# Kernel optimization log

Hardware: AMD Instinct MI355X
Metric: run time of the kernel (lower is better)

Reference implementation:

```python
import jax, jax.numpy as jnp
from jax import lax
import numpy as np

B, H, W, D_MODEL = 2, 64, 64, 192
D_INNER, D_STATE, DT_RANK = 384, 16, 12
L = H * W
LN_EPS = 1e-5


def setup_inputs() -> dict:
    ks = jax.random.split(jax.random.key(0), 12)
    rng = np.random.default_rng(0)
    perm = rng.permutation(L).astype(np.int32)

    def p(i, shape, scale=0.02):
        return jax.random.normal(ks[i], shape, dtype=jnp.float32) * scale

    return {
        "x": jax.random.normal(ks[0], (B, H, W, D_MODEL), dtype=jnp.float32),
        "condition": jax.random.normal(ks[1], (B, H, W, D_MODEL), dtype=jnp.float32),
        "W_in": p(2, (2 * D_INNER, D_MODEL)),
        "W_con": p(3, (D_INNER, D_MODEL)),
        "conv_w": p(4, (D_INNER, 1, 3, 3)),
        "conv_b": jnp.zeros((D_INNER,), jnp.float32),
        "con_conv_w": p(5, (D_INNER, 1, 3, 3)),
        "con_conv_b": jnp.zeros((D_INNER,), jnp.float32),
        "x_proj_w": p(6, (DT_RANK + 2 * D_STATE, D_INNER)),
        "dt_proj_w": p(7, (D_INNER, DT_RANK)),
        "dt_proj_b": p(8, (D_INNER,), 0.1),
        "A_logs": jnp.tile(jnp.log(jnp.arange(1, D_STATE + 1, dtype=jnp.float32))[None, :], (D_INNER, 1)),
        "Ds": jnp.ones((D_INNER,), jnp.float32),
        "ln_w": jnp.ones((D_INNER,), jnp.float32),
        "ln_b": jnp.zeros((D_INNER,), jnp.float32),
        "W_out": p(9, (D_MODEL, D_INNER)),
        "scan_path": jnp.asarray(perm),
        "rev_scan_path": jnp.asarray(np.argsort(perm).astype(np.int32)),
    }


def _dwconv(x, w, b):
    # depthwise 3x3 conv, SAME padding; x: [B, C, H, W], w: [C, 1, 3, 3]
    y = lax.conv_general_dilated(x, w, (1, 1), "SAME",
                                 dimension_numbers=("NCHW", "OIHW", "NCHW"),
                                 feature_group_count=x.shape[1])
    return y + b[None, :, None, None]


def _selective_scan(u, delta, A, Bs, Cs, D):
    # u, delta: [B, D, L]; A: [D, N]; Bs, Cs: [B, N, L]; D: [D]
    dA = jnp.exp(jnp.einsum("bdl,dn->lbdn", delta, A))          # [L, B, D, N]
    dBu = jnp.einsum("bdl,bnl,bdl->lbdn", delta, Bs, u)          # [L, B, D, N]
    Ct = jnp.transpose(Cs, (2, 0, 1))                             # [L, B, N]
    h0 = jnp.zeros(dA.shape[1:], dA.dtype)

    def step(h, inp):
        a, b, c = inp
        h = a * h + b
        return h, jnp.einsum("bdn,bn->bd", h, c)

    _, ys = lax.scan(step, h0, (dA, dBu, Ct))                     # ys: [L, B, D]
    y = jnp.transpose(ys, (1, 2, 0))                              # [B, D, L]
    return y + u * D[None, :, None]


def _forward(x, condition, W_in, W_con, conv_w, conv_b, con_conv_w, con_conv_b,
             x_proj_w, dt_proj_w, dt_proj_b, A_logs, Ds, ln_w, ln_b, W_out,
             scan_path, rev_scan_path):
    b, h, w, _ = x.shape
    l = h * w
    xz = x @ W_in.T                                               # [B, H, W, 2*Din]
    xa, z = jnp.split(xz, 2, axis=-1)
    z = jax.nn.silu(z)
    c = condition @ W_con.T
    xa = jax.nn.silu(_dwconv(jnp.transpose(xa, (0, 3, 1, 2)), conv_w, conv_b))
    c = jax.nn.silu(_dwconv(jnp.transpose(c, (0, 3, 1, 2)), con_conv_w, con_conv_b))
    d = xa.shape[1]
    xs = xa.reshape(b, d, l)[:, :, scan_path]                     # forward_permutation, K=1
    cs = c.reshape(b, d, l)[:, :, scan_path]
    x_dbl = jnp.einsum("bdl,cd->bcl", xs + cs, x_proj_w)          # [B, R+2N, L]
    r, n = dt_proj_w.shape[1], A_logs.shape[1]
    dts = jnp.einsum("brl,dr->bdl", x_dbl[:, :r], dt_proj_w)
    Bs = x_dbl[:, r:r + n]
    Cs = x_dbl[:, r + n:]
    A = -jnp.exp(A_logs)
    delta = jax.nn.softplus(dts + dt_proj_b[None, :, None])       # delta_softplus=True
    y = _selective_scan(xs, delta, A, Bs, Cs, Ds)                 # [B, D, L]
    y = y[:, :, rev_scan_path]                                    # backward_permutation
    y = jnp.transpose(y, (0, 2, 1))                               # [B, L, D]
    mu = jnp.mean(y, axis=-1, keepdims=True)
    var = jnp.var(y, axis=-1, keepdims=True)
    y = (y - mu) * lax.rsqrt(var + LN_EPS) * ln_w + ln_b          # out_norm
    y = y.reshape(b, h, w, d) * z
    return y @ W_out.T                                            # out_proj (no bias)


def reference(x, condition, W_in, W_con, conv_w, conv_b, con_conv_w, con_conv_b,
              x_proj_w, dt_proj_w, dt_proj_b, A_logs, Ds, ln_w, ln_b, W_out,
              scan_path, rev_scan_path):
    return _forward(x, condition, W_in, W_con, conv_w, conv_b, con_conv_w,
                    con_conv_b, x_proj_w, dt_proj_w, dt_proj_b, A_logs, Ds,
                    ln_w, ln_b, W_out, scan_path, rev_scan_path)
```

## Files before the change

kernel.cpp:

```cpp
#include <hip/hip_runtime.h>
#include <math.h>

#define BB 2
#define HH 64
#define WW 64
#define DM 192
#define DI 384
#define NS 16
#define DTR 12
#define LL 4096
#define ROWS (BB*LL)
#define NCHUNK 128
#define LCHUNK 32
#define NCOMB 448
#define CSTRIDE ((size_t)BB * DI * 8)

typedef __attribute__((ext_vector_type(8))) short bf16x8;
typedef __attribute__((ext_vector_type(4))) float f32x4;

typedef __attribute__((address_space(3))) void        as3_void;
typedef __attribute__((address_space(1))) const void  as1_cvoid;

__device__ __forceinline__ void gl_lds16(const unsigned short* g, unsigned short* l) {
    __builtin_amdgcn_global_load_lds((as1_cvoid*)g, (as3_void*)l, 16, 0, 0);
}

#define WAITCNT_BARRIER(N)                                         \
    do {                                                           \
        asm volatile("s_waitcnt vmcnt(" #N ")" ::: "memory");      \
        __builtin_amdgcn_s_barrier();                              \
        asm volatile("" ::: "memory");                             \
    } while (0)

__device__ __forceinline__ float silu_f(float v) {
    return v / (1.0f + __expf(-v));
}

__device__ __forceinline__ unsigned short f2bf(float f) {
    union { float f; unsigned int u; } c; c.f = f;
    unsigned int u = c.u;
    u += 0x7fffu + ((u >> 16) & 1u);
    return (unsigned short)(u >> 16);
}
__device__ __forceinline__ float bf2f(unsigned short h) {
    union { unsigned int u; float f; } c; c.u = ((unsigned int)h) << 16;
    return c.f;
}

__device__ __forceinline__ bf16x8 f2bf8(float4 a, float4 b) {
    bf16x8 r;
    r[0] = (short)f2bf(a.x); r[1] = (short)f2bf(a.y);
    r[2] = (short)f2bf(a.z); r[3] = (short)f2bf(a.w);
    r[4] = (short)f2bf(b.x); r[5] = (short)f2bf(b.y);
    r[6] = (short)f2bf(b.z); r[7] = (short)f2bf(b.w);
    return r;
}

__global__ __launch_bounds__(256) void gemm_in(
    const float* __restrict__ x, const float* __restrict__ cond,
    const float* __restrict__ w_in, const float* __restrict__ w_con,
    const float* __restrict__ x_proj_w, const float* __restrict__ dt_w,
    const float* __restrict__ w_out,
    unsigned short* __restrict__ xa_bf, unsigned short* __restrict__ z_bf,
    unsigned short* __restrict__ c_bf,
    unsigned short* __restrict__ wcomb_bf, unsigned short* __restrict__ w_out_bf)
{
    const int y = blockIdx.y;
    __shared__ __align__(16) unsigned short sA[2 * 64 * 32];
    __shared__ __align__(16) unsigned short sB[2 * 64 * 32];

    if (y == 18) {
        const int base = blockIdx.x * 256 + threadIdx.x;
        for (int i = base; i < 18432; i += 32768) {
            float4 v = ((const float4*)w_out)[i];
            ushort4 o;
            o.x = f2bf(v.x); o.y = f2bf(v.y); o.z = f2bf(v.z); o.w = f2bf(v.w);
            ((ushort4*)w_out_bf)[i] = o;
        }
        for (int e = base; e < NCOMB * DI; e += 32768) {
            int row = e / DI, k = e - row * DI;
            float v = 0.f;
            if (row < 384) {
                const float* dw = dt_w + row * DTR;
                #pragma unroll
                for (int r = 0; r < DTR; ++r) v += dw[r] * x_proj_w[r * DI + k];
            } else if (row < 416) {
                v = x_proj_w[(12 + (row - 384)) * DI + k];
            }
            wcomb_bf[e] = f2bf(v);
        }
        return;
    }

    const int zz = (y >= 12) ? 1 : 0;
    const float* A = zz ? cond : x;
    const float* W = zz ? w_con : w_in;
    const int bn = (zz ? (y - 12) : y) * 64;
    const int bm = blockIdx.x * 64;

    const int tid  = threadIdx.x;
    const int wave = tid >> 6;
    const int lane = tid & 63;
    const int quad = lane >> 4;
    const int l16  = lane & 15;
    const int srow = tid >> 2;
    const int q4   = tid & 3;
    const int wcol = (q4 ^ ((srow >> 1) & 3)) * 8;
    const int rswz = (quad ^ ((l16 >> 1) & 3)) * 8;

    f32x4 acc[4];
    #pragma unroll
    for (int t = 0; t < 4; ++t) acc[t] = (f32x4)(0.f);

    const float* gA = &A[(size_t)(bm + srow) * DM + q4 * 8];
    const float* gB = &W[(size_t)(bn + srow) * DM + q4 * 8];

    float4 ra0 = *(const float4*)gA,        ra1 = *(const float4*)(gA + 4);
    float4 rb0 = *(const float4*)gB,        rb1 = *(const float4*)(gB + 4);
    *(bf16x8*)&sA[srow * 32 + wcol] = f2bf8(ra0, ra1);
    *(bf16x8*)&sB[srow * 32 + wcol] = f2bf8(rb0, rb1);
    ra0 = *(const float4*)(gA + 32); ra1 = *(const float4*)(gA + 36);
    rb0 = *(const float4*)(gB + 32); rb1 = *(const float4*)(gB + 36);

    const int ar = (wave * 16 + l16) * 32 + rswz;

    #pragma unroll
    for (int t = 0; t < 6; ++t) {
        __syncthreads();
        const unsigned short* cA = &sA[(t & 1) * 2048];
        const unsigned short* cB = &sB[(t & 1) * 2048];
        bf16x8 a = *(bf16x8*)&cA[ar];
        if (t + 1 < 6) {
            const int nb = (t + 1) & 1;
            *(bf16x8*)&sA[nb * 2048 + srow * 32 + wcol] = f2bf8(ra0, ra1);
            *(bf16x8*)&sB[nb * 2048 + srow * 32 + wcol] = f2bf8(rb0, rb1);
            if (t + 2 < 6) {
                const int k = (t + 2) * 32;
                ra0 = *(const float4*)(gA + k); ra1 = *(const float4*)(gA + k + 4);
                rb0 = *(const float4*)(gB + k); rb1 = *(const float4*)(gB + k + 4);
            }
        }
        #pragma unroll
        for (int n = 0; n < 4; ++n) {
            bf16x8 b = *(bf16x8*)&cB[(n * 16 + l16) * 32 + rswz];
            acc[n] = __builtin_amdgcn_mfma_f32_16x16x32_bf16(a, b, acc[n], 0, 0, 0);
        }
    }

    #pragma unroll
    for (int n = 0; n < 4; ++n) {
        int col = bn + n * 16 + l16;
        #pragma unroll
        for (int r = 0; r < 4; ++r) {
            int row = bm + wave * 16 + quad * 4 + r;
            float v = acc[n][r];
            if (zz == 0) {
                if (col < 384) xa_bf[(size_t)row * 384 + col] = f2bf(v);
                else           z_bf[(size_t)row * 384 + (col - 384)] = f2bf(silu_f(v));
            } else {
                c_bf[(size_t)row * 384 + col] = f2bf(v);
            }
        }
    }
}

__global__ __launch_bounds__(256) void gemm_comb(
    const unsigned short* __restrict__ A, const unsigned short* __restrict__ W,
    const float* __restrict__ bias, float* __restrict__ btct,
    unsigned short* __restrict__ du_lo)
{
    __shared__ __align__(16) unsigned short sA[4 * 64 * 32];
    __shared__ __align__(16) unsigned short sB[4 * 64 * 32];
    const int bm = blockIdx.x * 64;
    const int bn = blockIdx.y * 64;
    const int tid  = threadIdx.x;
    const int wave = tid >> 6;
    const int lane = tid & 63;
    const int quad = lane >> 4;
    const int l16  = lane & 15;
    const int srow = tid >> 2;
    const int scol = ((tid & 3) ^ ((tid >> 3) & 3)) * 8;
    const int rswz = (quad ^ ((l16 >> 1) & 3)) * 8;

    f32x4 acc[4];
    #pragma unroll
    for (int t = 0; t < 4; ++t) acc[t] = (f32x4)(0.f);

    const unsigned short* gA = &A[(size_t)(bm + srow) * DI + scol];
    const unsigned short* gB = &W[(size_t)(bn + srow) * DI + scol];

    #pragma unroll
    for (int p = 0; p < 3; ++p) {
        gl_lds16(gA + p * 32, &sA[p * 2048 + wave * 512]);
        gl_lds16(gB + p * 32, &sB[p * 2048 + wave * 512]);
    }
    WAITCNT_BARRIER(4);

    const int ar = (wave * 16 + l16) * 32 + rswz;

    #pragma unroll
    for (int t = 0; t < 12; ++t) {
        if (t + 3 < 12) {
            const int k = (t + 3) * 32, pb = (t + 3) & 3;
            gl_lds16(gA + k, &sA[pb * 2048 + wave * 512]);
            gl_lds16(gB + k, &sB[pb * 2048 + wave * 512]);
        }
        const unsigned short* cA = &sA[(t & 3) * 2048];
        const unsigned short* cB = &sB[(t & 3) * 2048];
        bf16x8 a = *(bf16x8*)&cA[ar];
        #pragma unroll
        for (int n = 0; n < 4; ++n) {
            bf16x8 b = *(bf16x8*)&cB[(n * 16 + l16) * 32 + rswz];
            acc[n] = __builtin_amdgcn_mfma_f32_16x16x32_bf16(a, b, acc[n], 0, 0, 0);
        }
        if (t < 11) {
            if (t + 3 < 12)      WAITCNT_BARRIER(4);
            else if (t + 2 < 12) WAITCNT_BARRIER(2);
            else                 WAITCNT_BARRIER(0);
        }
    }

    #pragma unroll
    for (int n = 0; n < 4; ++n) {
        int col = bn + n * 16 + l16;
        #pragma unroll
        for (int r = 0; r < 4; ++r) {
            int row = bm + wave * 16 + quad * 4 + r;
            float v = acc[n][r];
            if (col < 384) {
                float a = v + bias[col];
                float sp = (a > 20.f) ? a : log1pf(__expf(a));
                du_lo[((size_t)row * 384 + col) * 2] = f2bf(sp);
            } else if (col < 416) {
                int idx = col - 384;
                int pos = (idx < 16) ? ((idx & 7) * 4 + (idx >> 3))
                                     : (((idx - 16) & 7) * 4 + 2 + ((idx - 16) >> 3));
                btct[(size_t)row * 32 + pos] = v;
            }
        }
    }
}

__global__ __launch_bounds__(256) void gemm_out_fused(
    const unsigned short* __restrict__ yt, const unsigned short* __restrict__ z,
    const float* __restrict__ ln_w, const float* __restrict__ ln_b,
    const unsigned short* __restrict__ W, float* __restrict__ out)
{
    __shared__ __align__(16) unsigned short sA[32 * 392];
    const int bm = blockIdx.x * 32;
    const int bn = blockIdx.y * 64;
    const int tid = threadIdx.x;
    const int r2  = tid >> 3;
    const int q8  = tid & 7;
    const int b   = bm >> 12;
    const int l   = (bm & (LL - 1)) + r2;

    const unsigned short* yrow = yt + ((size_t)(b * LL + l)) * DI;
    const unsigned short* zrow = z  + ((size_t)(b * LL + l)) * DI;

    bf16x8 yv[6];
    float s = 0.f, s2 = 0.f;
    #pragma unroll
    for (int i = 0; i < 6; ++i) {
        yv[i] = *(const bf16x8*)&yrow[i * 64 + q8 * 8];
        #pragma unroll
        for (int e = 0; e < 8; ++e) {
            float f = bf2f((unsigned short)yv[i][e]);
            s += f; s2 += f * f;
        }
    }
    s  += __shfl_xor(s, 1);  s  += __shfl_xor(s, 2);  s  += __shfl_xor(s, 4);
    s2 += __shfl_xor(s2, 1); s2 += __shfl_xor(s2, 2); s2 += __shfl_xor(s2, 4);
    const float mu  = s * (1.0f / DI);
    const float inv = rsqrtf(s2 * (1.0f / DI) - mu * mu + 1e-5f);

    #pragma unroll
    for (int i = 0; i < 6; ++i) {
        int c = i * 64 + q8 * 8;
        bf16x8 zv = *(const bf16x8*)&zrow[c];
        float4 wa = *(const float4*)&ln_w[c];
        float4 wb = *(const float4*)&ln_w[c + 4];
        float4 ba = *(const float4*)&ln_b[c];
        float4 bb = *(const float4*)&ln_b[c + 4];
        bf16x8 o;
        o[0] = (short)f2bf(((bf2f((unsigned short)yv[i][0]) - mu) * inv * wa.x + ba.x) * bf2f((unsigned short)zv[0]));
        o[1] = (short)f2bf(((bf2f((unsigned short)yv[i][1]) - mu) * inv * wa.y + ba.y) * bf2f((unsigned short)zv[1]));
        o[2] = (short)f2bf(((bf2f((unsigned short)yv[i][2]) - mu) * inv * wa.z + ba.z) * bf2f((unsigned short)zv[2]));
        o[3] = (short)f2bf(((bf2f((unsigned short)yv[i][3]) - mu) * inv * wa.w + ba.w) * bf2f((unsigned short)zv[3]));
        o[4] = (short)f2bf(((bf2f((unsigned short)yv[i][4]) - mu) * inv * wb.x + bb.x) * bf2f((unsigned short)zv[4]));
        o[5] = (short)f2bf(((bf2f((unsigned short)yv[i][5]) - mu) * inv * wb.y + bb.y) * bf2f((unsigned short)zv[5]));
        o[6] = (short)f2bf(((bf2f((unsigned short)yv[i][6]) - mu) * inv * wb.z + bb.z) * bf2f((unsigned short)zv[6]));
        o[7] = (short)f2bf(((bf2f((unsigned short)yv[i][7]) - mu) * inv * wb.w + bb.w) * bf2f((unsigned short)zv[7]));
        *(bf16x8*)&sA[r2 * 392 + c] = o;
    }

    __syncthreads();

    const int wave = tid >> 6;
    const int lane = tid & 63;
    const int quad = lane >> 4;
    const int l16  = lane & 15;
    const int rf   = wave >> 1;
    const int np   = (wave & 1) * 2;

    f32x4 acc[2];
    acc[0] = (f32x4)(0.f); acc[1] = (f32x4)(0.f);

    const unsigned short* bp0 = &W[(size_t)(bn + np * 16 + l16) * DI + quad * 8];
    const unsigned short* bp1 = bp0 + (size_t)16 * DI;
    const int abase = (rf * 16 + l16) * 392 + quad * 8;

    #pragma unroll
    for (int t = 0; t < 12; ++t) {
        bf16x8 a  = *(bf16x8*)&sA[abase + t * 32];
        bf16x8 b0 = *(const bf16x8*)(bp0 + t * 32);
        bf16x8 b1 = *(const bf16x8*)(bp1 + t * 32);
        acc[0] = __builtin_amdgcn_mfma_f32_16x16x32_bf16(a, b0, acc[0], 0, 0, 0);
        acc[1] = __builtin_amdgcn_mfma_f32_16x16x32_bf16(a, b1, acc[1], 0, 0, 0);
    }

    #pragma unroll
    for (int k = 0; k < 2; ++k) {
        int col = bn + (np + k) * 16 + l16;
        #pragma unroll
        for (int rr = 0; rr < 4; ++rr) {
            int row = bm + rf * 16 + quad * 4 + rr;
            out[(size_t)row * DM + col] = acc[k][rr];
        }
    }
}

__global__ __launch_bounds__(256) void dwconv2_scatter(
    const unsigned short* __restrict__ xin, const unsigned short* __restrict__ cin,
    const float* __restrict__ wx, const float* __restrict__ bx,
    const float* __restrict__ wc, const float* __restrict__ bc,
    const int* __restrict__ rev_scan_path,
    unsigned short* __restrict__ du_hi,
    unsigned short* __restrict__ s_bf)
{
    const int tile = blockIdx.x;
    const int c0   = blockIdx.y * 32;
    const int b    = blockIdx.z;
    const int h0 = (tile >> 3) * 8, w0 = (tile & 7) * 8;
    __shared__ float smx[10 * 10 * 32];
    __shared__ float smc[10 * 10 * 32];
    __shared__ int   jtile[64];

    for (int idx = threadIdx.x; idx < 800; idx += 256) {
        int pix = idx >> 3, cq = (idx & 7) * 4;
        int py = pix / 10, px = pix - py * 10;
        int gh = h0 + py - 1, gw = w0 + px - 1;
        float4 fx = make_float4(0.f, 0.f, 0.f, 0.f);
        float4 fc = make_float4(0.f, 0.f, 0.f, 0.f);
        if (gh >= 0 && gh < 64 && gw >= 0 && gw < 64) {
            size_t g = ((size_t)(b * LL + gh * 64 + gw)) * DI + c0 + cq;
            ushort4 vx = *(const ushort4*)&xin[g];
            ushort4 vc = *(const ushort4*)&cin[g];
            fx = make_float4(bf2f(vx.x), bf2f(vx.y), bf2f(vx.z), bf2f(vx.w));
            fc = make_float4(bf2f(vc.x), bf2f(vc.y), bf2f(vc.z), bf2f(vc.w));
        }
        *(float4*)&smx[pix * 32 + cq] = fx;
        *(float4*)&smc[pix * 32 + cq] = fc;
    }
    if (threadIdx.x < 64) {
        int l = (h0 + (threadIdx.x >> 3)) * 64 + (w0 + (threadIdx.x & 7));
        jtile[threadIdx.x] = rev_scan_path[l];
    }
    __syncthreads();

    const int ch = threadIdx.x & 31;
    const int pq = threadIdx.x >> 5;
    float wrx[9], wrc[9];
    #pragma unroll
    for (int k = 0; k < 9; ++k) {
        wrx[k] = wx[(c0 + ch) * 9 + k];
        wrc[k] = wc[(c0 + ch) * 9 + k];
    }
    const float bvx = bx[c0 + ch];
    const float bvc = bc[c0 + ch];

    #pragma unroll
    for (int i = 0; i < 8; ++i) {
        int p  = pq * 8 + i;
        int ph = p >> 3, pw = p & 7;
        float ax = bvx, ac = bvc;
        #pragma unroll
        for (int ki = 0; ki < 3; ++ki)
            #pragma unroll
            for (int kj = 0; kj < 3; ++kj) {
                int si = ((ph + ki) * 10 + (pw + kj)) * 32 + ch;
                ax += wrx[ki * 3 + kj] * smx[si];
                ac += wrc[ki * 3 + kj] * smc[si];
            }
        float xv = silu_f(ax);
        float sv = xv + silu_f(ac);
        size_t o = ((size_t)(b * LL + jtile[p])) * DI + c0 + ch;
        du_hi[o * 2 + 1] = f2bf(xv);
        s_bf[o]          = f2bf(sv);
    }
}

__global__ __launch_bounds__(256) void scan_chunkA(
    const unsigned int* __restrict__ du, const float* __restrict__ btct,
    const float* __restrict__ A_logs,
    float* __restrict__ chunkA, float* __restrict__ chunkB)
{
    const int c = blockIdx.x;
    const int g = blockIdx.y;
    const int b = blockIdx.z;
    const int t = threadIdx.x;
    const int grp = t >> 3, p = t & 7;
    const int d = g * 32 + grp;
    const float Av0 = -__expf(A_logs[d * NS + p]);
    const float Av1 = -__expf(A_logs[d * NS + p + 8]);
    const int j0 = c * LCHUNK;

    const unsigned int* dul = du + ((size_t)b * LL + j0) * DI + d;
    const float2*       bl  = (const float2*)btct + ((size_t)b * LL + j0) * 16 + p * 2;

    float h0 = 0.f, h1 = 0.f, Sd = 0.f;
    unsigned int duv[4]; float2 bv[4];
    #pragma unroll
    for (int q = 0; q < 4; ++q) {
        duv[q] = dul[(size_t)q * DI]; bv[q] = bl[(size_t)q * 16];
    }
    for (int j = 0; j < LCHUNK; j += 4) {
        unsigned int ndu[4]; float2 nb[4];
        if (j + 4 < LCHUNK) {
            #pragma unroll
            for (int q = 0; q < 4; ++q) {
                int jj = j + 4 + q;
                ndu[q] = dul[(size_t)jj * DI]; nb[q] = bl[(size_t)jj * 16];
            }
        }
        #pragma unroll
        for (int q = 0; q < 4; ++q) {
            float dv = bf2f((unsigned short)(duv[q] & 0xffff));
            float uv = bf2f((unsigned short)(duv[q] >> 16));
            float e0 = __expf(dv * Av0);
            float e1 = __expf(dv * Av1);
            float duu = dv * uv;
            h0 = e0 * h0 + bv[q].x * duu;
            h1 = e1 * h1 + bv[q].y * duu;
            Sd += dv;
        }
        #pragma unroll
        for (int q = 0; q < 4; ++q) { duv[q]=ndu[q]; bv[q]=nb[q]; }
    }
    size_t idx = (size_t)c * CSTRIDE + ((size_t)b * DI + d) * 8 + p;
    ((float2*)chunkA)[idx] = make_float2(__expf(Sd * Av0), __expf(Sd * Av1));
    ((float2*)chunkB)[idx] = make_float2(h0, h1);
}

__global__ __launch_bounds__(256) void scan_chunkC(
    const unsigned int* __restrict__ du, const float* __restrict__ btct,
    const float* __restrict__ A_logs, const float* __restrict__ Ds,
    const float* __restrict__ chunkA, const float* __restrict__ chunkB,
    const int* __restrict__ scan_path,
    unsigned short* __restrict__ yt)
{
    const int c = blockIdx.x;
    const int g = blockIdx.y;
    const int b = blockIdx.z;
    const int t = threadIdx.x;
    const int grp = t >> 3, p = t & 7;
    const int d = g * 32 + grp;
    const float Av0 = -__expf(A_logs[d * NS + p]);
    const float Av1 = -__expf(A_logs[d * NS + p + 8]);
    const float Dv = Ds[d];
    const int j0 = c * LCHUNK;

    const unsigned int* dul = du + ((size_t)b * LL + j0) * DI + d;
    const float4*       bcl = (const float4*)btct + ((size_t)b * LL + j0) * 8 + p;
    unsigned short* ytb = yt + (size_t)b * LL * DI + d;

    const size_t off = ((size_t)b * DI + d) * 8 + p;
    const float2* A2 = (const float2*)chunkA;
    const float2* B2 = (const float2*)chunkB;
    float h0 = 0.f, h1 = 0.f, P0 = 1.f, P1 = 1.f;
    for (int i = c - 1; i >= 0; --i) {
        size_t ix = (size_t)i * CSTRIDE + off;
        float2 a = A2[ix], bv = B2[ix];
        h0 += P0 * bv.x;  h1 += P1 * bv.y;
        P0 *= a.x;        P1 *= a.y;
        if (fmaxf(fabsf(P0), fabsf(P1)) < 1e-30f) break;
    }

    unsigned int duv[4]; float4 bc[4];
    #pragma unroll
    for (int q = 0; q < 4; ++q) {
        duv[q] = dul[(size_t)q * DI]; bc[q] = bcl[(size_t)q * 8];
    }
    for (int j = 0; j < LCHUNK; j += 4) {
        unsigned int ndu[4]; float4 nbc[4];
        if (j + 4 < LCHUNK) {
            #pragma unroll
            for (int q = 0; q < 4; ++q) {
                int jj = j + 4 + q;
                ndu[q] = dul[(size_t)jj * DI]; nbc[q] = bcl[(size_t)jj * 8];
            }
        }
        #pragma unroll
        for (int q = 0; q < 4; ++q) {
            float dv = bf2f((unsigned short)(duv[q] & 0xffff));
            float uv = bf2f((unsigned short)(duv[q] >> 16));
            float e0 = __expf(dv * Av0);
            float e1 = __expf(dv * Av1);
            float duu = dv * uv;
            h0 = e0 * h0 + bc[q].x * duu;
            h1 = e1 * h1 + bc[q].y * duu;
            float acc = h0 * bc[q].z + h1 * bc[q].w;
            acc += __shfl_xor(acc, 4, 8);
            acc += __shfl_xor(acc, 2, 8);
            acc += __shfl_xor(acc, 1, 8);
            if (p == 0) {
                int lsp = scan_path[j0 + j + q];
                ytb[(size_t)lsp * DI] = f2bf(acc + uv * Dv);
            }
        }
        #pragma unroll
        for (int q = 0; q < 4; ++q) { duv[q]=ndu[q]; bc[q]=nbc[q]; }
    }
}

extern "C" void kernel_launch(void* const* d_in, const int* in_sizes, int n_in,
                              void* d_out, int out_size, void* d_ws, size_t ws_size,
                              hipStream_t stream) {
    const float* x          = (const float*)d_in[0];
    const float* cond       = (const float*)d_in[1];
    const float* W_in       = (const float*)d_in[2];
    const float* W_con      = (const float*)d_in[3];
    const float* conv_w     = (const float*)d_in[4];
    const float* conv_b     = (const float*)d_in[5];
    const float* con_conv_w = (const float*)d_in[6];
    const float* con_conv_b = (const float*)d_in[7];
    const float* x_proj_w   = (const float*)d_in[8];
    const float* dt_proj_w  = (const float*)d_in[9];
    const float* dt_proj_b  = (const float*)d_in[10];
    const float* A_logs     = (const float*)d_in[11];
    const float* Ds         = (const float*)d_in[12];
    const float* ln_w       = (const float*)d_in[13];
    const float* ln_b       = (const float*)d_in[14];
    const float* W_out      = (const float*)d_in[15];
    const int*   scan_path  = (const int*)d_in[16];
    const int*   rev_path   = (const int*)d_in[17];

    float* ws = (float*)d_ws;
    const size_t S  = (size_t)BB * LL * DI;
    const size_t SC = (size_t)NCHUNK * BB * DI * NS;
    float* ytslab  = ws + 0 * S;
    float* zslab   = ws + 1 * S;
    float* duslab  = ws + 2 * S;
    float* btct    = ws + 3 * S;
    float* chunkA  = btct + (size_t)BB * LL * 32;
    float* chunkB  = chunkA + SC;
    float* bfpool  = chunkB + SC;

    unsigned short* yt_bf    = (unsigned short*)ytslab;
    unsigned short* z_bf     = (unsigned short*)zslab;
    unsigned int*   du       = (unsigned int*)duslab;
    unsigned short* s_bf     = (unsigned short*)bfpool;
    unsigned short* xa_bf    = s_bf + (size_t)ROWS * DI;
    unsigned short* c_bf     = xa_bf + (size_t)ROWS * DI;
    unsigned short* w_out_bf = c_bf + (size_t)ROWS * DI;
    unsigned short* wcomb_bf = w_out_bf + 192 * DI;

    gemm_in<<<dim3(ROWS / 64, 19), 256, 0, stream>>>(
        x, cond, W_in, W_con, x_proj_w, dt_proj_w, W_out,
        xa_bf, z_bf, c_bf, wcomb_bf, w_out_bf);
    dwconv2_scatter<<<dim3(64, 12, BB), 256, 0, stream>>>(
        xa_bf, c_bf, conv_w, conv_b, con_conv_w, con_conv_b,
        rev_path, (unsigned short*)du, s_bf);
    gemm_comb<<<dim3(ROWS / 64, NCOMB / 64), 256, 0, stream>>>(
        s_bf, wcomb_bf, dt_proj_b, btct, (unsigned short*)du);
    scan_chunkA<<<dim3(NCHUNK, DI / 32, BB), 256, 0, stream>>>(
        du, btct, A_logs, chunkA, chunkB);
    scan_chunkC<<<dim3(NCHUNK, DI / 32, BB), 256, 0, stream>>>(
        du, btct, A_logs, Ds, chunkA, chunkB, scan_path, yt_bf);
    gemm_out_fused<<<dim3(ROWS / 32, DM / 64), 256, 0, stream>>>(
        yt_bf, z_bf, ln_w, ln_b, w_out_bf, (float*)d_out);
}
```

Measured before the change: 197.9 us.

## Rewrite input and combined GEMMs to load fragments directly into registers

Both gemm_in and gemm_comb drop the LDS staging and double-buffered pipelines. Each wave now loads its A fragments once into registers and streams B fragments straight from global memory into MFMA calls, working on 32-row tiles with wide column strips (384 columns per block for gemm_in, 224 for gemm_comb). This removes LDS traffic and barriers and cuts the number of blocks. In exchange, B rows are re-read from global/L2 by every block with no sharing inside a block, register use grows, and latency hiding now relies on the compiler scheduling the loads.

After: 288.2 us. +45.6%, slower.

```diff
diff --git a/kernel.cpp b/kernel.cpp
--- a/kernel.cpp
+++ b/kernel.cpp
@@ -25,13 +25,6 @@
     __builtin_amdgcn_global_load_lds((as1_cvoid*)g, (as3_void*)l, 16, 0, 0);
 }
 
-#define WAITCNT_BARRIER(N)                                         \
-    do {                                                           \
-        asm volatile("s_waitcnt vmcnt(" #N ")" ::: "memory");      \
-        __builtin_amdgcn_s_barrier();                              \
-        asm volatile("" ::: "memory");                             \
-    } while (0)
-
 __device__ __forceinline__ float silu_f(float v) {
     return v / (1.0f + __expf(-v));
 }
@@ -66,18 +59,16 @@
     unsigned short* __restrict__ wcomb_bf, unsigned short* __restrict__ w_out_bf)
 {
     const int y = blockIdx.y;
-    __shared__ __align__(16) unsigned short sA[2 * 64 * 32];
-    __shared__ __align__(16) unsigned short sB[2 * 64 * 32];
-
-    if (y == 18) {
+
+    if (y == 3) {
         const int base = blockIdx.x * 256 + threadIdx.x;
-        for (int i = base; i < 18432; i += 32768) {
+        for (int i = base; i < 18432; i += 65536) {
             float4 v = ((const float4*)w_out)[i];
             ushort4 o;
             o.x = f2bf(v.x); o.y = f2bf(v.y); o.z = f2bf(v.z); o.w = f2bf(v.w);
             ((ushort4*)w_out_bf)[i] = o;
         }
-        for (int e = base; e < NCOMB * DI; e += 32768) {
+        for (int e = base; e < NCOMB * DI; e += 65536) {
             int row = e / DI, k = e - row * DI;
             float v = 0.f;
             if (row < 384) {
@@ -92,74 +83,62 @@
         return;
     }
 
-    const int zz = (y >= 12) ? 1 : 0;
-    const float* A = zz ? cond : x;
-    const float* W = zz ? w_con : w_in;
-    const int bn = (zz ? (y - 12) : y) * 64;
-    const int bm = blockIdx.x * 64;
+    const float* A = (y == 2) ? cond : x;
+    const float* W = (y == 2) ? w_con : w_in;
+    const int colbase = (y == 1) ? 384 : 0;
 
     const int tid  = threadIdx.x;
     const int wave = tid >> 6;
     const int lane = tid & 63;
     const int quad = lane >> 4;
     const int l16  = lane & 15;
-    const int srow = tid >> 2;
-    const int q4   = tid & 3;
-    const int wcol = (q4 ^ ((srow >> 1) & 3)) * 8;
-    const int rswz = (quad ^ ((l16 >> 1) & 3)) * 8;
-
-    f32x4 acc[4];
-    #pragma unroll
-    for (int t = 0; t < 4; ++t) acc[t] = (f32x4)(0.f);
-
-    const float* gA = &A[(size_t)(bm + srow) * DM + q4 * 8];
-    const float* gB = &W[(size_t)(bn + srow) * DM + q4 * 8];
-
-    float4 ra0 = *(const float4*)gA,        ra1 = *(const float4*)(gA + 4);
-    float4 rb0 = *(const float4*)gB,        rb1 = *(const float4*)(gB + 4);
-    *(bf16x8*)&sA[srow * 32 + wcol] = f2bf8(ra0, ra1);
-    *(bf16x8*)&sB[srow * 32 + wcol] = f2bf8(rb0, rb1);
-    ra0 = *(const float4*)(gA + 32); ra1 = *(const float4*)(gA + 36);
-    rb0 = *(const float4*)(gB + 32); rb1 = *(const float4*)(gB + 36);
-
-    const int ar = (wave * 16 + l16) * 32 + rswz;
-
-    #pragma unroll
-    for (int t = 0; t < 6; ++t) {
-        __syncthreads();
-        const unsigned short* cA = &sA[(t & 1) * 2048];
-        const unsigned short* cB = &sB[(t & 1) * 2048];
-        bf16x8 a = *(bf16x8*)&cA[ar];
-        if (t + 1 < 6) {
-            const int nb = (t + 1) & 1;
-            *(bf16x8*)&sA[nb * 2048 + srow * 32 + wcol] = f2bf8(ra0, ra1);
-            *(bf16x8*)&sB[nb * 2048 + srow * 32 + wcol] = f2bf8(rb0, rb1);
-            if (t + 2 < 6) {
-                const int k = (t + 2) * 32;
-                ra0 = *(const float4*)(gA + k); ra1 = *(const float4*)(gA + k + 4);
-                rb0 = *(const float4*)(gB + k); rb1 = *(const float4*)(gB + k + 4);
-            }
-        }
-        #pragma unroll
-        for (int n = 0; n < 4; ++n) {
-            bf16x8 b = *(bf16x8*)&cB[(n * 16 + l16) * 32 + rswz];
-            acc[n] = __builtin_amdgcn_mfma_f32_16x16x32_bf16(a, b, acc[n], 0, 0, 0);
-        }
-    }
-
-    #pragma unroll
-    for (int n = 0; n < 4; ++n) {
-        int col = bn + n * 16 + l16;
+    const int rf   = wave >> 1;
+    const int q    = wave & 1;
+    const int bm   = blockIdx.x * 32;
+
+    const float* gA = &A[(size_t)(bm + rf * 16 + l16) * DM + quad * 8];
+    bf16x8 af0 = f2bf8(*(const float4*)(gA +   0), *(const float4*)(gA +   4));
+    bf16x8 af1 = f2bf8(*(const float4*)(gA +  32), *(const float4*)(gA +  36));
+    bf16x8 af2 = f2bf8(*(const float4*)(gA +  64), *(const float4*)(gA +  68));
+    bf16x8 af3 = f2bf8(*(const float4*)(gA +  96), *(const float4*)(gA + 100));
+    bf16x8 af4 = f2bf8(*(const float4*)(gA + 128), *(const float4*)(gA + 132));
+    bf16x8 af5 = f2bf8(*(const float4*)(gA + 160), *(const float4*)(gA + 164));
+
+    f32x4 acc[12];
+    #pragma unroll
+    for (int i = 0; i < 12; ++i) acc[i] = (f32x4)(0.f);
+
+    const unsigned short* gB =
+        &((const unsigned short*)nullptr)[0];
+    (void)gB;
+
+    #pragma unroll
+    for (int cf = 0; cf < 12; ++cf) {
+        const float* bp = &W[(size_t)(colbase + q * 192 + cf * 16 + l16) * DM + quad * 8];
+        bf16x8 b0 = f2bf8(*(const float4*)(bp +   0), *(const float4*)(bp +   4));
+        bf16x8 b1 = f2bf8(*(const float4*)(bp +  32), *(const float4*)(bp +  36));
+        bf16x8 b2 = f2bf8(*(const float4*)(bp +  64), *(const float4*)(bp +  68));
+        bf16x8 b3 = f2bf8(*(const float4*)(bp +  96), *(const float4*)(bp + 100));
+        bf16x8 b4 = f2bf8(*(const float4*)(bp + 128), *(const float4*)(bp + 132));
+        bf16x8 b5 = f2bf8(*(const float4*)(bp + 160), *(const float4*)(bp + 164));
+        acc[cf] = __builtin_amdgcn_mfma_f32_16x16x32_bf16(af0, b0, acc[cf], 0, 0, 0);
+        acc[cf] = __builtin_amdgcn_mfma_f32_16x16x32_bf16(af1, b1, acc[cf], 0, 0, 0);
+        acc[cf] = __builtin_amdgcn_mfma_f32_16x16x32_bf16(af2, b2, acc[cf], 0, 0, 0);
+        acc[cf] = __builtin_amdgcn_mfma_f32_16x16x32_bf16(af3, b3, acc[cf], 0, 0, 0);
+        acc[cf] = __builtin_amdgcn_mfma_f32_16x16x32_bf16(af4, b4, acc[cf], 0, 0, 0);
+        acc[cf] = __builtin_amdgcn_mfma_f32_16x16x32_bf16(af5, b5, acc[cf], 0, 0, 0);
+    }
+
+    #pragma unroll
+    for (int cf = 0; cf < 12; ++cf) {
+        int colq = q * 192 + cf * 16 + l16;
         #pragma unroll
         for (int r = 0; r < 4; ++r) {
-            int row = bm + wave * 16 + quad * 4 + r;
-            float v = acc[n][r];
-            if (zz == 0) {
-                if (col < 384) xa_bf[(size_t)row * 384 + col] = f2bf(v);
-                else           z_bf[(size_t)row * 384 + (col - 384)] = f2bf(silu_f(v));
-            } else {
-                c_bf[(size_t)row * 384 + col] = f2bf(v);
-            }
+            int row = bm + rf * 16 + quad * 4 + r;
+            float v = acc[cf][r];
+            if (y == 0)      xa_bf[(size_t)row * 384 + colq] = f2bf(v);
+            else if (y == 1) z_bf[(size_t)row * 384 + colq]  = f2bf(silu_f(v));
+            else             c_bf[(size_t)row * 384 + colq]  = f2bf(v);
         }
     }
 }
@@ -169,64 +148,42 @@
     const float* __restrict__ bias, float* __restrict__ btct,
     unsigned short* __restrict__ du_lo)
 {
-    __shared__ __align__(16) unsigned short sA[4 * 64 * 32];
-    __shared__ __align__(16) unsigned short sB[4 * 64 * 32];
-    const int bm = blockIdx.x * 64;
-    const int bn = blockIdx.y * 64;
     const int tid  = threadIdx.x;
     const int wave = tid >> 6;
     const int lane = tid & 63;
     const int quad = lane >> 4;
     const int l16  = lane & 15;
-    const int srow = tid >> 2;
-    const int scol = ((tid & 3) ^ ((tid >> 3) & 3)) * 8;
-    const int rswz = (quad ^ ((l16 >> 1) & 3)) * 8;
-
-    f32x4 acc[4];
-    #pragma unroll
-    for (int t = 0; t < 4; ++t) acc[t] = (f32x4)(0.f);
-
-    const unsigned short* gA = &A[(size_t)(bm + srow) * DI + scol];
-    const unsigned short* gB = &W[(size_t)(bn + srow) * DI + scol];
-
-    #pragma unroll
-    for (int p = 0; p < 3; ++p) {
-        gl_lds16(gA + p * 32, &sA[p * 2048 + wave * 512]);
-        gl_lds16(gB + p * 32, &sB[p * 2048 + wave * 512]);
-    }
-    WAITCNT_BARRIER(4);
-
-    const int ar = (wave * 16 + l16) * 32 + rswz;
-
-    #pragma unroll
-    for (int t = 0; t < 12; ++t) {
-        if (t + 3 < 12) {
-            const int k = (t + 3) * 32, pb = (t + 3) & 3;
-            gl_lds16(gA + k, &sA[pb * 2048 + wave * 512]);
-            gl_lds16(gB + k, &sB[pb * 2048 + wave * 512]);
-        }
-        const unsigned short* cA = &sA[(t & 3) * 2048];
-        const unsigned short* cB = &sB[(t & 3) * 2048];
-        bf16x8 a = *(bf16x8*)&cA[ar];
-        #pragma unroll
-        for (int n = 0; n < 4; ++n) {
-            bf16x8 b = *(bf16x8*)&cB[(n * 16 + l16) * 32 + rswz];
-            acc[n] = __builtin_amdgcn_mfma_f32_16x16x32_bf16(a, b, acc[n], 0, 0, 0);
-        }
-        if (t < 11) {
-            if (t + 3 < 12)      WAITCNT_BARRIER(4);
-            else if (t + 2 < 12) WAITCNT_BARRIER(2);
-            else                 WAITCNT_BARRIER(0);
-        }
-    }
-
-    #pragma unroll
-    for (int n = 0; n < 4; ++n) {
-        int col = bn + n * 16 + l16;
+    const int rf   = wave >> 1;
+    const int q    = wave & 1;
+    const int bm   = blockIdx.x * 32;
+    const int cbase = blockIdx.y * 224 + q * 112;
+
+    const unsigned short* gA = &A[(size_t)(bm + rf * 16 + l16) * DI + quad * 8];
+    bf16x8 af[12];
+    #pragma unroll
+    for (int t = 0; t < 12; ++t) af[t] = *(const bf16x8*)(gA + t * 32);
+
+    f32x4 acc[7];
+    #pragma unroll
+    for (int i = 0; i < 7; ++i) acc[i] = (f32x4)(0.f);
+
+    #pragma unroll
+    for (int cf = 0; cf < 7; ++cf) {
+        const unsigned short* bp = &W[(size_t)(cbase + cf * 16 + l16) * DI + quad * 8];
+        #pragma unroll
+        for (int t = 0; t < 12; ++t) {
+            bf16x8 b = *(const bf16x8*)(bp + t * 32);
+            acc[cf] = __builtin_amdgcn_mfma_f32_16x16x32_bf16(af[t], b, acc[cf], 0, 0, 0);
+        }
+    }
+
+    #pragma unroll
+    for (int cf = 0; cf < 7; ++cf) {
+        int col = cbase + cf * 16 + l16;
         #pragma unroll
         for (int r = 0; r < 4; ++r) {
-            int row = bm + wave * 16 + quad * 4 + r;
-            float v = acc[n][r];
+            int row = bm + rf * 16 + quad * 4 + r;
+            float v = acc[cf][r];
             if (col < 384) {
                 float a = v + bias[col];
                 float sp = (a > 20.f) ? a : log1pf(__expf(a));
@@ -565,13 +522,13 @@
     unsigned short* w_out_bf = c_bf + (size_t)ROWS * DI;
     unsigned short* wcomb_bf = w_out_bf + 192 * DI;
 
-    gemm_in<<<dim3(ROWS / 64, 19), 256, 0, stream>>>(
+    gemm_in<<<dim3(ROWS / 32, 4), 256, 0, stream>>>(
         x, cond, W_in, W_con, x_proj_w, dt_proj_w, W_out,
         xa_bf, z_bf, c_bf, wcomb_bf, w_out_bf);
     dwconv2_scatter<<<dim3(64, 12, BB), 256, 0, stream>>>(
         xa_bf, c_bf, conv_w, conv_b, con_conv_w, con_conv_b,
         rev_path, (unsigned short*)du, s_bf);
-    gemm_comb<<<dim3(ROWS / 64, NCOMB / 64), 256, 0, stream>>>(
+    gemm_comb<<<dim3(ROWS / 32, 2), 256, 0, stream>>>(
         s_bf, wcomb_bf, dt_proj_b, btct, (unsigned short*)du);
     scan_chunkA<<<dim3(NCHUNK, DI / 32, BB), 256, 0, stream>>>(
         du, btct, A_logs, chunkA, chunkB);
```
